# Kernel tuning notes

Hardware: AMD Instinct MI355X
Metric: run time of the kernel (lower is better)

## Reference

```python
import jax, jax.numpy as jnp
import numpy as np

IN_CAPS = 128      # number of memory capsules (rows of m)
NUM_CAPS = 5       # n_class
DIM_CAPS = 153     # comp_dim // n_class = 768 // 5
IN_DIM = 768       # comp_dim
NQ = 256           # number of query samples
NUM_ROUTING = 3
BETA = 1.0         # config['Model']['temperature']
EPS = 1e-8


def _pearsonr(x, y):
    # Pearson correlation along last dim (broadcasts over leading dims).
    xm = x - x.mean(axis=-1, keepdims=True)
    ym = y - y.mean(axis=-1, keepdims=True)
    num = (xm * ym).sum(axis=-1)
    den = jnp.sqrt((xm * xm).sum(axis=-1)) * jnp.sqrt((ym * ym).sum(axis=-1))
    return num / (den + EPS)


def _squash(s):
    # capsule squash along last dim
    n2 = (s * s).sum(axis=-1, keepdims=True)
    return (n2 / (1.0 + n2)) * s / jnp.sqrt(n2 + EPS)


def setup_inputs() -> dict:
    key = jax.random.key(0)
    k1, k2, k3 = jax.random.split(key, 3)
    m = jax.random.normal(k1, (IN_CAPS, IN_DIM), dtype=jnp.float32)
    q = jax.random.normal(k2, (NQ, IN_DIM), dtype=jnp.float32)
    W = jax.random.normal(k3, (IN_DIM, NUM_CAPS * DIM_CAPS), dtype=jnp.float32) * 0.02
    b = jnp.zeros((NUM_CAPS * DIM_CAPS,), dtype=jnp.float32)
    return {"m": m, "q": q, "W": W, "b": b}


def reference(m, q, W, b):
    sg = jax.lax.stop_gradient
    # projections -> capsule preactivations
    hat_m = (m @ W + b).reshape(IN_CAPS, NUM_CAPS, DIM_CAPS)          # [I,C,D]
    hat_q = (q @ W + b).reshape(-1, NUM_CAPS, DIM_CAPS)               # [Q,C,D]
    Qn = hat_q.shape[0]
    tmp_m = sg(hat_m)[None, :, :, :]                                   # [1,I,C,D] (broadcast over Q)
    tmp_q = sg(hat_q)[:, None, :, :]                                   # [Q,1,C,D]

    a = jnp.zeros((Qn, IN_CAPS, NUM_CAPS), dtype=hat_q.dtype)          # routing logits
    p = jnp.tanh(_pearsonr(tmp_m, tmp_q))                              # [Q,I,C]

    for _ in range(NUM_ROUTING - 1):
        d = jax.nn.softmax(a / BETA, axis=2)                           # [Q,I,C]
        dsp = d + p
        hat_v = (tmp_m * dsp[..., None]).sum(axis=1)                   # [Q,C,D]
        v = _squash(hat_v)
        m_dot_v = (tmp_m * v[:, None, :, :]).sum(axis=-1)              # [Q,I,C]
        a = a + p * m_dot_v
        tmp_q = (tmp_q + v[:, None, :, :]) * 0.5                       # [Q,I,C,D]
        p = jnp.tanh(_pearsonr(tmp_m, tmp_q))

    d = jax.nn.softmax(a / BETA, axis=2)
    dsp = sg(d + p)                                                    # routing coeffs detached
    hat_v = (hat_m[None, :, :, :] * dsp[..., None]).sum(axis=1)        # grad flows via hat_m only
    q_prime = _squash(hat_v).reshape(Qn, -1)                           # [Q, C*D]
    return q_prime
```

## Files before the change

### kernel.cpp

```cpp
#include <hip/hip_runtime.h>
#include <hip/hip_bf16.h>

#define I_CAPS 128
#define N_CAPS 5
#define D_CAPS 153
#define D_PAD  160
#define MLD    800
#define IN_DIM 768
#define NQ     256
#define CD     765
#define NPAIR  640
#define EPSF   1e-8f
#define KHALF  384

typedef __hip_bfloat16 bf16;

__device__ __forceinline__ float wred(float x) {
#pragma unroll
  for (int off = 32; off; off >>= 1) x += __shfl_down(x, off, 64);
  return x;
}

__device__ __forceinline__ float tanh_fast(float x) {
  float t = __expf(-2.f * fabsf(x));
  float r = (1.f - t) / (1.f + t);
  return copysignf(r, x);
}

__global__ void classify_kernel(const unsigned* __restrict__ m_u32,
                                int* __restrict__ flag) {
  int lane = threadIdx.x & 63;
  unsigned u = m_u32[lane];
  int e = (u >> 7) & 0xFF;
  int hit = (e >= 118 && e <= 134) ? 1 : 0;
  unsigned long long mask = __ballot(hit);
  if (lane == 0) *flag = (__popcll(mask) >= 48) ? 1 : 0;
}

template <bool ISB>
__device__ __forceinline__ float ld_in(const void* p, long idx) {
  if (ISB) return __bfloat162float(((const bf16*)p)[idx]);
  return ((const float*)p)[idx];
}

template <bool ISB>
__device__ void gemm_body(const void* m, const void* q, const void* W,
                          const void* b, float* hat_m, float* hat_q) {
  __shared__ float As[8][KHALF];
  const int tx = threadIdx.x, ty = threadIdx.y;
  const int t = ty * 64 + tx;
  const int row0 = blockIdx.y * 8;
  const int k0 = blockIdx.z * KHALF;

  if (ISB) {
    for (int e = t; e < 8 * KHALF; e += 256) {
      int rr = e / KHALF, kk = e - rr * KHALF;
      int row = row0 + rr;
      As[rr][kk] = (row < I_CAPS)
                       ? ld_in<true>(m, (long)row * IN_DIM + k0 + kk)
                       : ld_in<true>(q, (long)(row - I_CAPS) * IN_DIM + k0 + kk);
    }
  } else {
    for (int e = t; e < 8 * (KHALF / 4); e += 256) {
      int rr = e / (KHALF / 4), k4 = e - rr * (KHALF / 4);
      int row = row0 + rr;
      const float* src = (row < I_CAPS)
                             ? (const float*)m + (long)row * IN_DIM
                             : (const float*)q + (long)(row - I_CAPS) * IN_DIM;
      *(float4*)&As[rr][k4 * 4] = *(const float4*)(src + k0 + k4 * 4);
    }
  }
  __syncthreads();

  const int col = blockIdx.x * 64 + tx;
  const int colc = (col < CD) ? col : (CD - 1);
  const int r0 = ty * 2, r1 = r0 + 1;

  float a0a = 0.f, a0b = 0.f, a1a = 0.f, a1b = 0.f;
#pragma unroll 2
  for (int k = 0; k < KHALF; k += 8) {
    const float4 A0a = *(const float4*)&As[r0][k];
    const float4 A0b = *(const float4*)&As[r0][k + 4];
    const float4 A1a = *(const float4*)&As[r1][k];
    const float4 A1b = *(const float4*)&As[r1][k + 4];
    float w0 = ld_in<ISB>(W, (long)(k0 + k + 0) * CD + colc);
    float w1 = ld_in<ISB>(W, (long)(k0 + k + 1) * CD + colc);
    float w2 = ld_in<ISB>(W, (long)(k0 + k + 2) * CD + colc);
    float w3 = ld_in<ISB>(W, (long)(k0 + k + 3) * CD + colc);
    float w4 = ld_in<ISB>(W, (long)(k0 + k + 4) * CD + colc);
    float w5 = ld_in<ISB>(W, (long)(k0 + k + 5) * CD + colc);
    float w6 = ld_in<ISB>(W, (long)(k0 + k + 6) * CD + colc);
    float w7 = ld_in<ISB>(W, (long)(k0 + k + 7) * CD + colc);
    a0a = fmaf(A0a.x, w0, a0a); a0b = fmaf(A0a.y, w1, a0b);
    a0a = fmaf(A0a.z, w2, a0a); a0b = fmaf(A0a.w, w3, a0b);
    a0a = fmaf(A0b.x, w4, a0a); a0b = fmaf(A0b.y, w5, a0b);
    a0a = fmaf(A0b.z, w6, a0a); a0b = fmaf(A0b.w, w7, a0b);
    a1a = fmaf(A1a.x, w0, a1a); a1b = fmaf(A1a.y, w1, a1b);
    a1a = fmaf(A1a.z, w2, a1a); a1b = fmaf(A1a.w, w3, a1b);
    a1a = fmaf(A1b.x, w4, a1a); a1b = fmaf(A1b.y, w5, a1b);
    a1a = fmaf(A1b.z, w6, a1a); a1b = fmaf(A1b.w, w7, a1b);
  }

  if (col < CD) {
    float p0 = a0a + a0b;
    float p1 = a1a + a1b;
    if (blockIdx.z == 0) {
      float bias = ld_in<ISB>(b, col);
      p0 += bias;
      p1 += bias;
    }
    int c = col / D_CAPS, d = col - c * D_CAPS;
    int ra = row0 + r0, rb = row0 + r1;
    float* d0 = (ra < I_CAPS) ? &hat_m[ra * MLD + c * D_PAD + d]
                              : &hat_q[(ra - I_CAPS) * CD + col];
    float* d1 = (rb < I_CAPS) ? &hat_m[rb * MLD + c * D_PAD + d]
                              : &hat_q[(rb - I_CAPS) * CD + col];
    atomicAdd(d0, p0);
    atomicAdd(d1, p1);
  }
}

__global__ __launch_bounds__(256, 4)
void gemm_kernel(const void* m, const void* q, const void* W, const void* b,
                 const int* __restrict__ flag,
                 float* __restrict__ hat_m, float* __restrict__ hat_q) {
  if (*flag)
    gemm_body<true>(m, q, W, b, hat_m, hat_q);
  else
    gemm_body<false>(m, q, W, b, hat_m, hat_q);
}

__global__ __launch_bounds__(256)
void stats_kernel(const float* __restrict__ hat_m,
                  float* __restrict__ mean_m, float* __restrict__ ssm) {
  const int wave = threadIdx.x >> 6, lane = threadIdx.x & 63;
  const int pair = blockIdx.x * 4 + wave;
  const int i = pair / N_CAPS, c = pair - i * N_CAPS;
  const float* hm = hat_m + i * MLD + c * D_PAD;
  float s = 0.f, s2 = 0.f;
  for (int d = lane; d < D_CAPS; d += 64) {
    float x = hm[d];
    s += x;
    s2 = fmaf(x, x, s2);
  }
  s = wred(s);
  s2 = wred(s2);
  if (lane == 0) {
    float mu = s * (1.f / D_CAPS);
    mean_m[pair] = mu;
    ssm[pair] = fmaxf(s2 - (float)D_CAPS * mu * mu, 0.f);
  }
}

__global__ __launch_bounds__(1024, 4)
void routing_kernel(const float* __restrict__ hat_m,
                    const float* __restrict__ hat_q,
                    const float* __restrict__ mean_m,
                    const float* __restrict__ ssm,
                    const int* __restrict__ flag,
                    void* __restrict__ out_v) {
  __shared__ float tq[N_CAPS * D_PAD], vv[N_CAPS * D_PAD];
  __shared__ float aa[NPAIR], pp[NPAIR], dsp[NPAIR], sdot[NPAIR];
  __shared__ float smm[NPAIR], sss[NPAIR];
  __shared__ float meanq[N_CAPS], ssq[N_CAPS], sscale[N_CAPS];

  const int tid = threadIdx.x;
  const int qi = blockIdx.x;
  const int w = tid >> 6, lane = tid & 63;
  const int g = tid >> 3, sub = tid & 7;
  const float* hq = hat_q + qi * CD;
  const float* hm = hat_m + g * MLD;

  for (int l = tid; l < N_CAPS * D_PAD; l += 1024) {
    int c = l / D_PAD, d = l - c * D_PAD;
    tq[l] = (d < D_CAPS) ? hq[c * D_CAPS + d] : 0.f;
    vv[l] = 0.f;
  }
  if (tid < NPAIR) {
    aa[tid] = 0.f;
    smm[tid] = mean_m[tid];
    sss[tid] = ssm[tid];
  }
  __syncthreads();

  auto qstats = [&]() {
    if (w < N_CAPS) {
      const int c = w;
      float s = 0.f, s2 = 0.f;
      for (int d = lane; d < D_CAPS; d += 64) {
        float x = tq[c * D_PAD + d];
        s += x;
        s2 = fmaf(x, x, s2);
      }
      s = wred(s);
      s2 = wred(s2);
      if (lane == 0) {
        float mu = s * (1.f / D_CAPS);
        meanq[c] = mu;
        ssq[c] = fmaxf(s2 - (float)D_CAPS * mu * mu, 0.f);
      }
    }
  };

  #define DOT5(vec, A0, A1, A2, A3, A4)                                   \
    {                                                                     \
      _Pragma("unroll 2") for (int jj = 0; jj < 5; ++jj) {                \
        int d = jj * 32 + sub * 4;                                        \
        float4 h0 = *(const float4*)(hm + 0 * D_PAD + d);                 \
        float4 h1 = *(const float4*)(hm + 1 * D_PAD + d);                 \
        float4 h2 = *(const float4*)(hm + 2 * D_PAD + d);                 \
        float4 h3 = *(const float4*)(hm + 3 * D_PAD + d);                 \
        float4 h4 = *(const float4*)(hm + 4 * D_PAD + d);                 \
        float4 t0 = *(const float4*)(vec + 0 * D_PAD + d);                \
        float4 t1 = *(const float4*)(vec + 1 * D_PAD + d);                \
        float4 t2 = *(const float4*)(vec + 2 * D_PAD + d);                \
        float4 t3 = *(const float4*)(vec + 3 * D_PAD + d);                \
        float4 t4 = *(const float4*)(vec + 4 * D_PAD + d);                \
        A0 = fmaf(h0.x, t0.x, A0); A0 = fmaf(h0.y, t0.y, A0);             \
        A0 = fmaf(h0.z, t0.z, A0); A0 = fmaf(h0.w, t0.w, A0);             \
        A1 = fmaf(h1.x, t1.x, A1); A1 = fmaf(h1.y, t1.y, A1);             \
        A1 = fmaf(h1.z, t1.z, A1); A1 = fmaf(h1.w, t1.w, A1);             \
        A2 = fmaf(h2.x, t2.x, A2); A2 = fmaf(h2.y, t2.y, A2);             \
        A2 = fmaf(h2.z, t2.z, A2); A2 = fmaf(h2.w, t2.w, A2);             \
        A3 = fmaf(h3.x, t3.x, A3); A3 = fmaf(h3.y, t3.y, A3);             \
        A3 = fmaf(h3.z, t3.z, A3); A3 = fmaf(h3.w, t3.w, A3);             \
        A4 = fmaf(h4.x, t4.x, A4); A4 = fmaf(h4.y, t4.y, A4);             \
        A4 = fmaf(h4.z, t4.z, A4); A4 = fmaf(h4.w, t4.w, A4);             \
      }                                                                   \
      _Pragma("unroll") for (int off = 1; off < 8; off <<= 1) {           \
        A0 += __shfl_xor(A0, off, 64);                                    \
        A1 += __shfl_xor(A1, off, 64);                                    \
        A2 += __shfl_xor(A2, off, 64);                                    \
        A3 += __shfl_xor(A3, off, 64);                                    \
        A4 += __shfl_xor(A4, off, 64);                                    \
      }                                                                   \
    }

  auto sel5 = [&](float A0, float A1, float A2, float A3, float A4) {
    float r = A0;
    r = (sub == 1) ? A1 : r;
    r = (sub == 2) ? A2 : r;
    r = (sub == 3) ? A3 : r;
    r = (sub == 4) ? A4 : r;
    return r;
  };

  auto init_S_p = [&]() {
    float A0 = 0.f, A1 = 0.f, A2 = 0.f, A3 = 0.f, A4 = 0.f;
    DOT5(tq, A0, A1, A2, A3, A4);
    if (sub < N_CAPS) {
      float acc = sel5(A0, A1, A2, A3, A4);
      int pair = g * N_CAPS + sub;
      sdot[pair] = acc;
      float num = acc - (float)D_CAPS * smm[pair] * meanq[sub];
      float den = sqrtf(sss[pair]) * sqrtf(ssq[sub]) + EPSF;
      pp[pair] = tanh_fast(num / den);
    }
  };

  auto mdot_aa = [&]() {
    float A0 = 0.f, A1 = 0.f, A2 = 0.f, A3 = 0.f, A4 = 0.f;
    DOT5(vv, A0, A1, A2, A3, A4);
    if (sub < N_CAPS) {
      float acc = sel5(A0, A1, A2, A3, A4);
      int pair = g * N_CAPS + sub;
      float mdv = sscale[sub] * acc;
      aa[pair] += pp[pair] * mdv;
      sdot[pair] = 0.5f * (sdot[pair] + mdv);
    }
  };

  auto p_from_S = [&]() {
    if (tid < NPAIR) {
      int c = tid - (tid / N_CAPS) * N_CAPS;
      float num = sdot[tid] - (float)D_CAPS * smm[tid] * meanq[c];
      float den = sqrtf(sss[tid]) * sqrtf(ssq[c]) + EPSF;
      pp[tid] = tanh_fast(num / den);
    }
  };

  auto softmax_dsp = [&]() {
    if (tid < I_CAPS) {
      float av[N_CAPS], ev[N_CAPS];
      float mx = -1e30f;
#pragma unroll
      for (int c = 0; c < N_CAPS; ++c) {
        av[c] = aa[tid * N_CAPS + c];
        mx = fmaxf(mx, av[c]);
      }
      float s = 0.f;
#pragma unroll
      for (int c = 0; c < N_CAPS; ++c) {
        ev[c] = __expf(av[c] - mx);
        s += ev[c];
      }
      float inv = 1.f / s;
#pragma unroll
      for (int c = 0; c < N_CAPS; ++c)
        dsp[tid * N_CAPS + c] = ev[c] * inv + pp[tid * N_CAPS + c];
    }
  };

  auto hat_v = [&]() {
    for (int cd = tid; cd < CD; cd += 1024) {
      int c = cd / D_CAPS, d = cd - c * D_CAPS;
      const float* col = hat_m + c * D_PAD + d;
      float b0 = 0.f, b1 = 0.f, b2 = 0.f, b3 = 0.f;
      float b4 = 0.f, b5 = 0.f, b6 = 0.f, b7 = 0.f;
#pragma unroll 4
      for (int i = 0; i < I_CAPS; i += 8) {
        b0 = fmaf(dsp[(i + 0) * N_CAPS + c], col[(i + 0) * MLD], b0);
        b1 = fmaf(dsp[(i + 1) * N_CAPS + c], col[(i + 1) * MLD], b1);
        b2 = fmaf(dsp[(i + 2) * N_CAPS + c], col[(i + 2) * MLD], b2);
        b3 = fmaf(dsp[(i + 3) * N_CAPS + c], col[(i + 3) * MLD], b3);
        b4 = fmaf(dsp[(i + 4) * N_CAPS + c], col[(i + 4) * MLD], b4);
        b5 = fmaf(dsp[(i + 5) * N_CAPS + c], col[(i + 5) * MLD], b5);
        b6 = fmaf(dsp[(i + 6) * N_CAPS + c], col[(i + 6) * MLD], b6);
        b7 = fmaf(dsp[(i + 7) * N_CAPS + c], col[(i + 7) * MLD], b7);
      }
      vv[c * D_PAD + d] = ((b0 + b1) + (b2 + b3)) + ((b4 + b5) + (b6 + b7));
    }
  };

  auto squash_scale = [&]() {
    if (w < N_CAPS) {
      const int c = w;
      float s2 = 0.f;
      for (int d = lane; d < D_CAPS; d += 64) {
        float x = vv[c * D_PAD + d];
        s2 = fmaf(x, x, s2);
      }
      s2 = wred(s2);
      if (lane == 0) sscale[c] = (s2 / (1.f + s2)) * rsqrtf(s2 + EPSF);
    }
  };

  qstats();
  __syncthreads();
  init_S_p();
  __syncthreads();

  for (int r = 0; r < 2; ++r) {
    softmax_dsp();
    __syncthreads();
    hat_v();
    __syncthreads();
    squash_scale();
    __syncthreads();
    mdot_aa();
    for (int cd = tid; cd < CD; cd += 1024) {
      int c = cd / D_CAPS, d = cd - c * D_CAPS;
      int l = c * D_PAD + d;
      tq[l] = 0.5f * (tq[l] + vv[l] * sscale[c]);
    }
    __syncthreads();
    qstats();
    __syncthreads();
    p_from_S();
    __syncthreads();
  }

  softmax_dsp();
  __syncthreads();
  hat_v();
  __syncthreads();
  squash_scale();
  __syncthreads();

  if (*flag == 0) {
    float* out = (float*)out_v;
    for (int cd = tid; cd < CD; cd += 1024) {
      int c = cd / D_CAPS, d = cd - c * D_CAPS;
      out[qi * CD + cd] = vv[c * D_PAD + d] * sscale[c];
    }
  } else {
    bf16* out = (bf16*)out_v;
    for (int cd = tid; cd < CD; cd += 1024) {
      int c = cd / D_CAPS, d = cd - c * D_CAPS;
      out[qi * CD + cd] = __float2bfloat16(vv[c * D_PAD + d] * sscale[c]);
    }
  }
  #undef DOT5
}

extern "C" void kernel_launch(void* const* d_in, const int* in_sizes, int n_in,
                              void* d_out, int out_size, void* d_ws, size_t ws_size,
                              hipStream_t stream) {
  const void *m = nullptr, *q = nullptr, *W = nullptr, *b = nullptr;
  for (int i = 0; i < n_in; ++i) {
    switch (in_sizes[i]) {
      case I_CAPS * IN_DIM: m = d_in[i]; break;
      case NQ * IN_DIM:     q = d_in[i]; break;
      case IN_DIM * CD:     W = d_in[i]; break;
      case CD:              b = d_in[i]; break;
      default: break;
    }
  }
  if (!m || !q || !W || !b) {
    m = d_in[0]; q = d_in[1]; W = d_in[2]; b = d_in[3];
  }

  int*   flag   = (int*)d_ws;
  float* mean_m = (float*)d_ws + 16;
  float* ssm    = mean_m + 640;
  float* hat_m  = ssm + 640;
  float* hat_q  = hat_m + I_CAPS * MLD;

  classify_kernel<<<1, 64, 0, stream>>>((const unsigned*)m, flag);
  hipMemsetAsync(hat_m, 0,
                 ((size_t)I_CAPS * MLD + (size_t)NQ * CD) * sizeof(float),
                 stream);
  gemm_kernel<<<dim3(12, 48, 2), dim3(64, 4), 0, stream>>>(m, q, W, b, flag,
                                                           hat_m, hat_q);
  stats_kernel<<<160, 256, 0, stream>>>(hat_m, mean_m, ssm);
  routing_kernel<<<NQ, 1024, 0, stream>>>(hat_m, hat_q, mean_m, ssm, flag,
                                          d_out);
}
```

Measured before the change: 127.9 us.

## Precompute per-capsule Gram matrix to replace routing hat_v and dot passes

Adds a gram_kernel that computes the 5 per-capsule 128x128 Gram matrices of hat_m. The routing iterations then get m·v, the squash norm and the updated query statistics from G·dsp and scalar recurrences, so the per-iteration hat_v reduction over hat_m and the tq update are dropped. Only the final iteration still forms hat_v explicitly. This removes most of the global hat_m traffic inside the routing loop, but it adds a kernel launch and 320 KB of G reads per query block, and the recurrence-based statistics may drift numerically.

```diff
diff --git a/kernel.cpp b/kernel.cpp
--- a/kernel.cpp
+++ b/kernel.cpp
@@ -152,9 +152,28 @@
   }
 }
 
+__global__ __launch_bounds__(128)
+void gram_kernel(const float* __restrict__ hat_m, float* __restrict__ G) {
+  const int c = blockIdx.x, j = blockIdx.y, i = threadIdx.x;
+  const float4* hi = (const float4*)(hat_m + i * MLD + c * D_PAD);
+  const float4* hj = (const float4*)(hat_m + j * MLD + c * D_PAD);
+  float a0 = 0.f, a1 = 0.f, a2 = 0.f, a3 = 0.f;
+#pragma unroll 8
+  for (int k = 0; k < 40; ++k) {
+    float4 x = hi[k];
+    float4 y = hj[k];
+    a0 = fmaf(x.x, y.x, a0);
+    a1 = fmaf(x.y, y.y, a1);
+    a2 = fmaf(x.z, y.z, a2);
+    a3 = fmaf(x.w, y.w, a3);
+  }
+  G[c * 16384 + j * 128 + i] = (a0 + a1) + (a2 + a3);
+}
+
 __global__ __launch_bounds__(1024, 4)
 void routing_kernel(const float* __restrict__ hat_m,
                     const float* __restrict__ hat_q,
+                    const float* __restrict__ Gmat,
                     const float* __restrict__ mean_m,
                     const float* __restrict__ ssm,
                     const int* __restrict__ flag,
@@ -162,7 +181,9 @@
   __shared__ float tq[N_CAPS * D_PAD], vv[N_CAPS * D_PAD];
   __shared__ float aa[NPAIR], pp[NPAIR], dsp[NPAIR], sdot[NPAIR];
   __shared__ float smm[NPAIR], sss[NPAIR];
-  __shared__ float meanq[N_CAPS], ssq[N_CAPS], sscale[N_CAPS];
+  __shared__ float meanq[N_CAPS], ssq[N_CAPS], sc_s[N_CAPS];
+  __shared__ float tsum_s[N_CAPS], t2_s[N_CAPS];
+  __shared__ float red[10][4];
 
   const int tid = threadIdx.x;
   const int qi = blockIdx.x;
@@ -174,7 +195,6 @@
   for (int l = tid; l < N_CAPS * D_PAD; l += 1024) {
     int c = l / D_PAD, d = l - c * D_PAD;
     tq[l] = (d < D_CAPS) ? hq[c * D_CAPS + d] : 0.f;
-    vv[l] = 0.f;
   }
   if (tid < NPAIR) {
     aa[tid] = 0.f;
@@ -183,101 +203,74 @@
   }
   __syncthreads();
 
-  auto qstats = [&]() {
-    if (w < N_CAPS) {
-      const int c = w;
-      float s = 0.f, s2 = 0.f;
-      for (int d = lane; d < D_CAPS; d += 64) {
-        float x = tq[c * D_PAD + d];
-        s += x;
-        s2 = fmaf(x, x, s2);
-      }
-      s = wred(s);
-      s2 = wred(s2);
-      if (lane == 0) {
-        float mu = s * (1.f / D_CAPS);
-        meanq[c] = mu;
-        ssq[c] = fmaxf(s2 - (float)D_CAPS * mu * mu, 0.f);
-      }
-    }
-  };
-
-  #define DOT5(vec, A0, A1, A2, A3, A4)                                   \
-    {                                                                     \
-      _Pragma("unroll 2") for (int jj = 0; jj < 5; ++jj) {                \
-        int d = jj * 32 + sub * 4;                                        \
-        float4 h0 = *(const float4*)(hm + 0 * D_PAD + d);                 \
-        float4 h1 = *(const float4*)(hm + 1 * D_PAD + d);                 \
-        float4 h2 = *(const float4*)(hm + 2 * D_PAD + d);                 \
-        float4 h3 = *(const float4*)(hm + 3 * D_PAD + d);                 \
-        float4 h4 = *(const float4*)(hm + 4 * D_PAD + d);                 \
-        float4 t0 = *(const float4*)(vec + 0 * D_PAD + d);                \
-        float4 t1 = *(const float4*)(vec + 1 * D_PAD + d);                \
-        float4 t2 = *(const float4*)(vec + 2 * D_PAD + d);                \
-        float4 t3 = *(const float4*)(vec + 3 * D_PAD + d);                \
-        float4 t4 = *(const float4*)(vec + 4 * D_PAD + d);                \
-        A0 = fmaf(h0.x, t0.x, A0); A0 = fmaf(h0.y, t0.y, A0);             \
-        A0 = fmaf(h0.z, t0.z, A0); A0 = fmaf(h0.w, t0.w, A0);             \
-        A1 = fmaf(h1.x, t1.x, A1); A1 = fmaf(h1.y, t1.y, A1);             \
-        A1 = fmaf(h1.z, t1.z, A1); A1 = fmaf(h1.w, t1.w, A1);             \
-        A2 = fmaf(h2.x, t2.x, A2); A2 = fmaf(h2.y, t2.y, A2);             \
-        A2 = fmaf(h2.z, t2.z, A2); A2 = fmaf(h2.w, t2.w, A2);             \
-        A3 = fmaf(h3.x, t3.x, A3); A3 = fmaf(h3.y, t3.y, A3);             \
-        A3 = fmaf(h3.z, t3.z, A3); A3 = fmaf(h3.w, t3.w, A3);             \
-        A4 = fmaf(h4.x, t4.x, A4); A4 = fmaf(h4.y, t4.y, A4);             \
-        A4 = fmaf(h4.z, t4.z, A4); A4 = fmaf(h4.w, t4.w, A4);             \
-      }                                                                   \
-      _Pragma("unroll") for (int off = 1; off < 8; off <<= 1) {           \
-        A0 += __shfl_xor(A0, off, 64);                                    \
-        A1 += __shfl_xor(A1, off, 64);                                    \
-        A2 += __shfl_xor(A2, off, 64);                                    \
-        A3 += __shfl_xor(A3, off, 64);                                    \
-        A4 += __shfl_xor(A4, off, 64);                                    \
-      }                                                                   \
-    }
-
-  auto sel5 = [&](float A0, float A1, float A2, float A3, float A4) {
-    float r = A0;
-    r = (sub == 1) ? A1 : r;
-    r = (sub == 2) ? A2 : r;
-    r = (sub == 3) ? A3 : r;
-    r = (sub == 4) ? A4 : r;
-    return r;
-  };
-
-  auto init_S_p = [&]() {
+  if (w < N_CAPS) {
+    const int c = w;
+    float s = 0.f, s2 = 0.f;
+    for (int d = lane; d < D_CAPS; d += 64) {
+      float x = tq[c * D_PAD + d];
+      s += x;
+      s2 = fmaf(x, x, s2);
+    }
+    s = wred(s);
+    s2 = wred(s2);
+    if (lane == 0) {
+      float mu = s * (1.f / D_CAPS);
+      tsum_s[c] = s;
+      t2_s[c] = s2;
+      meanq[c] = mu;
+      ssq[c] = fmaxf(s2 - (float)D_CAPS * mu * mu, 0.f);
+    }
+  }
+  __syncthreads();
+
+  {
     float A0 = 0.f, A1 = 0.f, A2 = 0.f, A3 = 0.f, A4 = 0.f;
-    DOT5(tq, A0, A1, A2, A3, A4);
+#pragma unroll 2
+    for (int jj = 0; jj < 5; ++jj) {
+      int d = jj * 32 + sub * 4;
+      float4 h0 = *(const float4*)(hm + 0 * D_PAD + d);
+      float4 h1 = *(const float4*)(hm + 1 * D_PAD + d);
+      float4 h2 = *(const float4*)(hm + 2 * D_PAD + d);
+      float4 h3 = *(const float4*)(hm + 3 * D_PAD + d);
+      float4 h4 = *(const float4*)(hm + 4 * D_PAD + d);
+      float4 t0 = *(const float4*)(tq + 0 * D_PAD + d);
+      float4 t1 = *(const float4*)(tq + 1 * D_PAD + d);
+      float4 t2 = *(const float4*)(tq + 2 * D_PAD + d);
+      float4 t3 = *(const float4*)(tq + 3 * D_PAD + d);
+      float4 t4 = *(const float4*)(tq + 4 * D_PAD + d);
+      A0 = fmaf(h0.x, t0.x, A0); A0 = fmaf(h0.y, t0.y, A0);
+      A0 = fmaf(h0.z, t0.z, A0); A0 = fmaf(h0.w, t0.w, A0);
+      A1 = fmaf(h1.x, t1.x, A1); A1 = fmaf(h1.y, t1.y, A1);
+      A1 = fmaf(h1.z, t1.z, A1); A1 = fmaf(h1.w, t1.w, A1);
+      A2 = fmaf(h2.x, t2.x, A2); A2 = fmaf(h2.y, t2.y, A2);
+      A2 = fmaf(h2.z, t2.z, A2); A2 = fmaf(h2.w, t2.w, A2);
+      A3 = fmaf(h3.x, t3.x, A3); A3 = fmaf(h3.y, t3.y, A3);
+      A3 = fmaf(h3.z, t3.z, A3); A3 = fmaf(h3.w, t3.w, A3);
+      A4 = fmaf(h4.x, t4.x, A4); A4 = fmaf(h4.y, t4.y, A4);
+      A4 = fmaf(h4.z, t4.z, A4); A4 = fmaf(h4.w, t4.w, A4);
+    }
+#pragma unroll
+    for (int off = 1; off < 8; off <<= 1) {
+      A0 += __shfl_xor(A0, off, 64);
+      A1 += __shfl_xor(A1, off, 64);
+      A2 += __shfl_xor(A2, off, 64);
+      A3 += __shfl_xor(A3, off, 64);
+      A4 += __shfl_xor(A4, off, 64);
+    }
     if (sub < N_CAPS) {
-      float acc = sel5(A0, A1, A2, A3, A4);
-      int pair = g * N_CAPS + sub;
-      sdot[pair] = acc;
-      float num = acc - (float)D_CAPS * smm[pair] * meanq[sub];
-      float den = sqrtf(sss[pair]) * sqrtf(ssq[sub]) + EPSF;
-      pp[pair] = tanh_fast(num / den);
-    }
-  };
-
-  auto mdot_aa = [&]() {
-    float A0 = 0.f, A1 = 0.f, A2 = 0.f, A3 = 0.f, A4 = 0.f;
-    DOT5(vv, A0, A1, A2, A3, A4);
-    if (sub < N_CAPS) {
-      float acc = sel5(A0, A1, A2, A3, A4);
-      int pair = g * N_CAPS + sub;
-      float mdv = sscale[sub] * acc;
-      aa[pair] += pp[pair] * mdv;
-      sdot[pair] = 0.5f * (sdot[pair] + mdv);
-    }
-  };
-
-  auto p_from_S = [&]() {
-    if (tid < NPAIR) {
-      int c = tid - (tid / N_CAPS) * N_CAPS;
-      float num = sdot[tid] - (float)D_CAPS * smm[tid] * meanq[c];
-      float den = sqrtf(sss[tid]) * sqrtf(ssq[c]) + EPSF;
-      pp[tid] = tanh_fast(num / den);
-    }
-  };
+      float acc = A0;
+      acc = (sub == 1) ? A1 : acc;
+      acc = (sub == 2) ? A2 : acc;
+      acc = (sub == 3) ? A3 : acc;
+      acc = (sub == 4) ? A4 : acc;
+      int ic = g * N_CAPS + sub;
+      sdot[ic] = acc;
+      float num = acc - (float)D_CAPS * smm[ic] * meanq[sub];
+      float den = sqrtf(sss[ic]) * sqrtf(ssq[sub]) + EPSF;
+      pp[ic] = tanh_fast(num / den);
+    }
+  }
+  __syncthreads();
 
   auto softmax_dsp = [&]() {
     if (tid < I_CAPS) {
@@ -301,86 +294,111 @@
     }
   };
 
-  auto hat_v = [&]() {
-    for (int cd = tid; cd < CD; cd += 1024) {
-      int c = cd / D_CAPS, d = cd - c * D_CAPS;
-      const float* col = hat_m + c * D_PAD + d;
-      float b0 = 0.f, b1 = 0.f, b2 = 0.f, b3 = 0.f;
-      float b4 = 0.f, b5 = 0.f, b6 = 0.f, b7 = 0.f;
-#pragma unroll 4
-      for (int i = 0; i < I_CAPS; i += 8) {
-        b0 = fmaf(dsp[(i + 0) * N_CAPS + c], col[(i + 0) * MLD], b0);
-        b1 = fmaf(dsp[(i + 1) * N_CAPS + c], col[(i + 1) * MLD], b1);
-        b2 = fmaf(dsp[(i + 2) * N_CAPS + c], col[(i + 2) * MLD], b2);
-        b3 = fmaf(dsp[(i + 3) * N_CAPS + c], col[(i + 3) * MLD], b3);
-        b4 = fmaf(dsp[(i + 4) * N_CAPS + c], col[(i + 4) * MLD], b4);
-        b5 = fmaf(dsp[(i + 5) * N_CAPS + c], col[(i + 5) * MLD], b5);
-        b6 = fmaf(dsp[(i + 6) * N_CAPS + c], col[(i + 6) * MLD], b6);
-        b7 = fmaf(dsp[(i + 7) * N_CAPS + c], col[(i + 7) * MLD], b7);
-      }
-      vv[c * D_PAD + d] = ((b0 + b1) + (b2 + b3)) + ((b4 + b5) + (b6 + b7));
-    }
-  };
-
-  auto squash_scale = [&]() {
-    if (w < N_CAPS) {
-      const int c = w;
-      float s2 = 0.f;
-      for (int d = lane; d < D_CAPS; d += 64) {
-        float x = vv[c * D_PAD + d];
-        s2 = fmaf(x, x, s2);
-      }
-      s2 = wred(s2);
-      if (lane == 0) sscale[c] = (s2 / (1.f + s2)) * rsqrtf(s2 + EPSF);
-    }
-  };
-
-  qstats();
-  __syncthreads();
-  init_S_p();
-  __syncthreads();
-
   for (int r = 0; r < 2; ++r) {
     softmax_dsp();
     __syncthreads();
-    hat_v();
+    float y = 0.f, sold = 0.f;
+    int cc = 0, ii = 0, ic = 0;
+    if (tid < NPAIR) {
+      cc = tid >> 7;
+      ii = tid & 127;
+      ic = ii * N_CAPS + cc;
+      const float* Gp = Gmat + cc * 16384 + ii;
+      float y0 = 0.f, y1 = 0.f;
+#pragma unroll 4
+      for (int j = 0; j < 128; j += 2) {
+        y0 = fmaf(Gp[j * 128], dsp[j * N_CAPS + cc], y0);
+        y1 = fmaf(Gp[(j + 1) * 128], dsp[(j + 1) * N_CAPS + cc], y1);
+      }
+      y = y0 + y1;
+      sold = sdot[ic];
+      float dmy = dsp[ic];
+      float n2p = dmy * y;
+      float vsp = dmy * ((float)D_CAPS * smm[ic]);
+      float sdp = dmy * sold;
+      n2p = wred(n2p);
+      vsp = wred(vsp);
+      sdp = wred(sdp);
+      if (lane == 0) {
+        red[w][0] = n2p;
+        red[w][1] = vsp;
+        red[w][2] = sdp;
+      }
+    }
     __syncthreads();
-    squash_scale();
+    if (tid < N_CAPS) {
+      float n2 = red[2 * tid][0] + red[2 * tid + 1][0];
+      float vs = red[2 * tid][1] + red[2 * tid + 1][1];
+      float sd = red[2 * tid][2] + red[2 * tid + 1][2];
+      float sc = (n2 / (1.f + n2)) * rsqrtf(n2 + EPSF);
+      sc_s[tid] = sc;
+      float ts = 0.5f * (tsum_s[tid] + sc * vs);
+      float t2 = 0.25f * (t2_s[tid] + 2.f * sc * sd + sc * sc * n2);
+      tsum_s[tid] = ts;
+      t2_s[tid] = t2;
+      float mu = ts * (1.f / D_CAPS);
+      meanq[tid] = mu;
+      ssq[tid] = fmaxf(t2 - (float)D_CAPS * mu * mu, 0.f);
+    }
     __syncthreads();
-    mdot_aa();
-    for (int cd = tid; cd < CD; cd += 1024) {
-      int c = cd / D_CAPS, d = cd - c * D_CAPS;
-      int l = c * D_PAD + d;
-      tq[l] = 0.5f * (tq[l] + vv[l] * sscale[c]);
+    if (tid < NPAIR) {
+      float mdv = sc_s[cc] * y;
+      aa[ic] += pp[ic] * mdv;
+      float snew = 0.5f * (sold + mdv);
+      sdot[ic] = snew;
+      float num = snew - (float)D_CAPS * smm[ic] * meanq[cc];
+      float den = sqrtf(sss[ic]) * sqrtf(ssq[cc]) + EPSF;
+      pp[ic] = tanh_fast(num / den);
     }
     __syncthreads();
-    qstats();
-    __syncthreads();
-    p_from_S();
-    __syncthreads();
   }
 
   softmax_dsp();
   __syncthreads();
-  hat_v();
-  __syncthreads();
-  squash_scale();
+  for (int cd = tid; cd < CD; cd += 1024) {
+    int c = cd / D_CAPS, d = cd - c * D_CAPS;
+    const float* col = hat_m + c * D_PAD + d;
+    float b0 = 0.f, b1 = 0.f, b2 = 0.f, b3 = 0.f;
+    float b4 = 0.f, b5 = 0.f, b6 = 0.f, b7 = 0.f;
+#pragma unroll 4
+    for (int i = 0; i < I_CAPS; i += 8) {
+      b0 = fmaf(dsp[(i + 0) * N_CAPS + c], col[(i + 0) * MLD], b0);
+      b1 = fmaf(dsp[(i + 1) * N_CAPS + c], col[(i + 1) * MLD], b1);
+      b2 = fmaf(dsp[(i + 2) * N_CAPS + c], col[(i + 2) * MLD], b2);
+      b3 = fmaf(dsp[(i + 3) * N_CAPS + c], col[(i + 3) * MLD], b3);
+      b4 = fmaf(dsp[(i + 4) * N_CAPS + c], col[(i + 4) * MLD], b4);
+      b5 = fmaf(dsp[(i + 5) * N_CAPS + c], col[(i + 5) * MLD], b5);
+      b6 = fmaf(dsp[(i + 6) * N_CAPS + c], col[(i + 6) * MLD], b6);
+      b7 = fmaf(dsp[(i + 7) * N_CAPS + c], col[(i + 7) * MLD], b7);
+    }
+    vv[c * D_PAD + d] = ((b0 + b1) + (b2 + b3)) + ((b4 + b5) + (b6 + b7));
+  }
+  __syncthreads();
+  if (w < N_CAPS) {
+    const int c = w;
+    float s2 = 0.f;
+    for (int d = lane; d < D_CAPS; d += 64) {
+      float x = vv[c * D_PAD + d];
+      s2 = fmaf(x, x, s2);
+    }
+    s2 = wred(s2);
+    if (lane == 0) sc_s[c] = (s2 / (1.f + s2)) * rsqrtf(s2 + EPSF);
+  }
   __syncthreads();
 
   if (*flag == 0) {
     float* out = (float*)out_v;
     for (int cd = tid; cd < CD; cd += 1024) {
       int c = cd / D_CAPS, d = cd - c * D_CAPS;
-      out[qi * CD + cd] = vv[c * D_PAD + d] * sscale[c];
+      out[qi * CD + cd] = vv[c * D_PAD + d] * sc_s[c];
     }
   } else {
     bf16* out = (bf16*)out_v;
     for (int cd = tid; cd < CD; cd += 1024) {
       int c = cd / D_CAPS, d = cd - c * D_CAPS;
-      out[qi * CD + cd] = __float2bfloat16(vv[c * D_PAD + d] * sscale[c]);
-    }
-  }
-  #undef DOT5
+      out[qi * CD + cd] = __float2bfloat16(vv[c * D_PAD + d] * sc_s[c]);
+    }
+  }
 }
 
 extern "C" void kernel_launch(void* const* d_in, const int* in_sizes, int n_in,
@@ -405,6 +423,7 @@
   float* ssm    = mean_m + 640;
   float* hat_m  = ssm + 640;
   float* hat_q  = hat_m + I_CAPS * MLD;
+  float* G      = hat_q + NQ * CD;
 
   classify_kernel<<<1, 64, 0, stream>>>((const unsigned*)m, flag);
   hipMemsetAsync(hat_m, 0,
@@ -413,6 +432,7 @@
   gemm_kernel<<<dim3(12, 48, 2), dim3(64, 4), 0, stream>>>(m, q, W, b, flag,
                                                            hat_m, hat_q);
   stats_kernel<<<160, 256, 0, stream>>>(hat_m, mean_m, ssm);
-  routing_kernel<<<NQ, 1024, 0, stream>>>(hat_m, hat_q, mean_m, ssm, flag,
+  gram_kernel<<<dim3(N_CAPS, I_CAPS), 128, 0, stream>>>(hat_m, G);
+  routing_kernel<<<NQ, 1024, 0, stream>>>(hat_m, hat_q, G, mean_m, ssm, flag,
                                           d_out);
 }
```

Result: faster. 121.1 us (-5.3%).
